# Performance work log

Measured on AMD Instinct MI355X. Metric: run time of the kernel, lower is better.

Reference implementation:

```python
import jax, jax.numpy as jnp
import numpy as np

GROUPS = 32
EPS = 1e-5


def group_norm(x, gamma, beta):
    B, C, D, H, W = x.shape
    xr = x.reshape(B, GROUPS, C // GROUPS, D, H, W)
    mean = xr.mean(axis=(2, 3, 4, 5), keepdims=True)
    var = xr.var(axis=(2, 3, 4, 5), keepdims=True)
    xn = (xr - mean) * jax.lax.rsqrt(var + EPS)
    xn = xn.reshape(B, C, D, H, W)
    return xn * gamma[None, :, None, None, None] + beta[None, :, None, None, None]


def conv1x1(h, w, b):
    # 1x1x1 Conv3d == channel matmul. w: [O, C], b: [O]
    return jnp.einsum('oc,bcdhw->bodhw', w, h) + b[None, :, None, None, None]


def setup_inputs() -> dict:
    key = jax.random.key(0)
    ks = jax.random.split(key, 10)
    B, C, D, H, W = 2, 128, 16, 16, 16
    x = jax.random.normal(ks[0], (B, C, D, H, W), dtype=jnp.float32)
    gn_w = jnp.ones((C,), dtype=jnp.float32)
    gn_b = jnp.zeros((C,), dtype=jnp.float32)
    # xavier_uniform for [C, C, 1, 1, 1] conv: fan_in = fan_out = C
    lim = float(np.sqrt(6.0 / (C + C)))
    wq = jax.random.uniform(ks[1], (C, C), jnp.float32, -lim, lim)
    wk = jax.random.uniform(ks[2], (C, C), jnp.float32, -lim, lim)
    wv = jax.random.uniform(ks[3], (C, C), jnp.float32, -lim, lim)
    wp = jax.random.uniform(ks[4], (C, C), jnp.float32, -lim, lim) * 1e-05
    bq = jnp.zeros((C,), jnp.float32)
    bk = jnp.zeros((C,), jnp.float32)
    bv = jnp.zeros((C,), jnp.float32)
    bp = jnp.zeros((C,), jnp.float32)
    return {"x": x, "gn_w": gn_w, "gn_b": gn_b, "wq": wq, "bq": bq,
            "wk": wk, "bk": bk, "wv": wv, "bv": bv, "wp": wp, "bp": bp}


def reference(x, gn_w, gn_b, wq, bq, wk, bk, wv, bv, wp, bp):
    B, C, D, H, W = x.shape
    N = D * H * W
    h = group_norm(x, gn_w, gn_b)
    q = conv1x1(h, wq, bq)
    k = conv1x1(h, wk, bk)
    v = conv1x1(h, wv, bv)
    q = q.transpose(0, 2, 3, 4, 1).reshape(B, N, C)   # [B, N, C]
    k = k.reshape(B, C, N)                            # [B, C, N]
    v = v.transpose(0, 2, 3, 4, 1).reshape(B, N, C)   # [B, N, C]
    w = jnp.einsum('bnc,bcm->bnm', q, k) * (C ** -0.5)  # [B, N, N]
    w = jax.nn.softmax(w, axis=-1)
    h = jnp.einsum('bnm,bmc->bnc', w, v)              # [B, N, C]
    h = h.reshape(B, D, H, W, C).transpose(0, 4, 1, 2, 3)
    h = conv1x1(h, wp, bp)
    return x + h
```

## Files before the change

### kernel.cpp

```cpp
#include <hip/hip_runtime.h>
#include <math.h>

#define CC 128
#define NN 4096
#define BB 2
#define NGROUPS 32
#define CPG 4
#define GSIZE (CPG*NN)
#define KSPLIT 16

typedef __attribute__((ext_vector_type(8))) __bf16 bf16x8;
typedef __attribute__((ext_vector_type(4))) float floatx4;

__device__ __forceinline__ unsigned short f2bf(float f) {
  union { float f; unsigned u; } v; v.f = f;
  unsigned r = v.u + 0x7fff + ((v.u >> 16) & 1);
  return (unsigned short)(r >> 16);
}
__device__ __forceinline__ float bf2f(unsigned short u) {
  return __uint_as_float(((unsigned)u) << 16);
}


__device__ __forceinline__ void stage_tile(const unsigned short* __restrict__ gtile,
                                           unsigned short* ltile, int w, int lane) {
  #pragma unroll
  for (int j = 0; j < 4; j++) {
    int off = (w*4 + j) * 512;
    __builtin_amdgcn_global_load_lds(
        (const __attribute__((address_space(1))) unsigned int*)(gtile + off + lane*8),
        (__attribute__((address_space(3))) unsigned int*)(ltile + off),
        16, 0, 0);
  }
}

__global__ void gn_stats_kernel(const float* __restrict__ x, float2* __restrict__ stats,
                                const float* __restrict__ wq, const float* __restrict__ wk,
                                const float* __restrict__ wv, const float* __restrict__ wp,
                                unsigned short* __restrict__ wqb, unsigned short* __restrict__ wkb,
                                unsigned short* __restrict__ wvb, unsigned short* __restrict__ wpb) {
  int t = threadIdx.x;
  if (blockIdx.x < 256) {
    int bid = blockIdx.x;
    const float4* base = (const float4*)(x + (size_t)bid * 4096);
    float4 v = base[t];
    float s  = v.x + v.y + v.z + v.w;
    float ss = v.x*v.x + v.y*v.y + v.z*v.z + v.w*v.w;
    #pragma unroll
    for (int off = 1; off < 64; off <<= 1) {
      s  += __shfl_xor(s, off);
      ss += __shfl_xor(ss, off);
    }
    __shared__ float sred[4], ssred[4];
    if ((t & 63) == 0) { sred[t >> 6] = s; ssred[t >> 6] = ss; }
    __syncthreads();
    if (t == 0)
      stats[bid] = make_float2(sred[0]+sred[1]+sred[2]+sred[3],
                               ssred[0]+ssred[1]+ssred[2]+ssred[3]);
  } else {
    const float sc = 0.08838834764831845f;
    int i = (blockIdx.x - 256) * 256 + t;
    int id = i >> 12, local = i & 4095;
    const float* src = id==0 ? wq : id==1 ? wk : id==2 ? wv : wp;
    unsigned short* dst = id==0 ? wqb : id==1 ? wkb : id==2 ? wvb : wpb;
    float s = (id == 0) ? sc : 1.0f;
    float4 v = ((const float4*)src)[local];
    unsigned p0 = (unsigned)f2bf(v.x*s) | ((unsigned)f2bf(v.y*s) << 16);
    unsigned p1 = (unsigned)f2bf(v.z*s) | ((unsigned)f2bf(v.w*s) << 16);
    ((uint2*)dst)[local] = make_uint2(p0, p1);
  }
}

__global__ __launch_bounds__(256, 2) void qkv_kernel(
    const float* __restrict__ x, const float2* __restrict__ stats,
    const float* __restrict__ gamma, const float* __restrict__ beta,
    const unsigned short* __restrict__ wqb, const unsigned short* __restrict__ wkb,
    const unsigned short* __restrict__ wvb,
    const float* __restrict__ bq, const float* __restrict__ bk, const float* __restrict__ bv,
    unsigned short* __restrict__ q, unsigned short* __restrict__ k, unsigned short* __restrict__ v) {
  int b = blockIdx.y, n0 = blockIdx.x * 16;
  __shared__ unsigned short hs[16][130];
  __shared__ unsigned short vs[16][136];
  __shared__ float gm[NGROUPS], gr[NGROUPS], aa[CC], ab[CC];
  int t = threadIdx.x;
  if (t < NGROUPS) {
    float su = 0.f, ssq = 0.f;
    #pragma unroll
    for (int j = 0; j < 4; j++) {
      float2 p = stats[(b*NGROUPS + t)*4 + j];
      su += p.x; ssq += p.y;
    }
    float mean = su * (1.0f/GSIZE);
    float var  = ssq * (1.0f/GSIZE) - mean*mean;
    gm[t] = mean;
    gr[t] = rsqrtf(var + 1e-5f);
  }
  __syncthreads();
  if (t < CC) {
    int g = t >> 2;
    float a = gr[g] * gamma[t];
    aa[t] = a;
    ab[t] = beta[t] - gm[g] * a;
  }
  __syncthreads();
  #pragma unroll
  for (int j = 0; j < 2; j++) {
    int idx = j*256 + t;
    int c = idx >> 2, n4 = idx & 3;
    float4 xv = *(const float4*)(x + ((size_t)b*CC + c)*NN + n0 + n4*4);
    float a = aa[c], bc = ab[c];
    hs[n4*4+0][c] = f2bf(a*xv.x + bc);
    hs[n4*4+1][c] = f2bf(a*xv.y + bc);
    hs[n4*4+2][c] = f2bf(a*xv.z + bc);
    hs[n4*4+3][c] = f2bf(a*xv.w + bc);
  }
  __syncthreads();
  int w = t >> 6, lane = t & 63, quad = lane >> 4, c = lane & 15;
  int o0 = w * 32;
  bf16x8 af[4];
  #pragma unroll
  for (int ks = 0; ks < 4; ks++)
    af[ks] = *(const bf16x8*)&hs[c][ks*32 + quad*8];
  floatx4 aq[2], ak[2], av[2];
  #pragma unroll
  for (int ct = 0; ct < 2; ct++) {
    aq[ct] = (floatx4){0.f,0.f,0.f,0.f};
    ak[ct] = (floatx4){0.f,0.f,0.f,0.f};
    av[ct] = (floatx4){0.f,0.f,0.f,0.f};
  }
  #pragma unroll
  for (int ks = 0; ks < 4; ks++) {
    #pragma unroll
    for (int ct = 0; ct < 2; ct++) {
      size_t woff = (size_t)(o0 + ct*16 + c)*CC + ks*32 + quad*8;
      bf16x8 bq8 = *(const bf16x8*)(wqb + woff);
      bf16x8 bk8 = *(const bf16x8*)(wkb + woff);
      bf16x8 bv8 = *(const bf16x8*)(wvb + woff);
      aq[ct] = __builtin_amdgcn_mfma_f32_16x16x32_bf16(af[ks], bq8, aq[ct], 0, 0, 0);
      ak[ct] = __builtin_amdgcn_mfma_f32_16x16x32_bf16(af[ks], bk8, ak[ct], 0, 0, 0);
      av[ct] = __builtin_amdgcn_mfma_f32_16x16x32_bf16(af[ks], bv8, av[ct], 0, 0, 0);
    }
  }
  {
    const float sc = 0.08838834764831845f;
    size_t base = (size_t)b*NN*CC + (size_t)blockIdx.x*2048 + w*512;
    #pragma unroll
    for (int ct = 0; ct < 2; ct++) {
      float bqi = bq[o0 + ct*16 + c] * sc;
      float bki = bk[o0 + ct*16 + c];
      #pragma unroll
      for (int r = 0; r < 4; r++) {
        int idx = (quad*4 + r)*32 + ct*16 + c;
        q[base + idx] = f2bf(aq[ct][r] + bqi);
        k[base + idx] = f2bf(ak[ct][r] + bki);
      }
    }
  }
  #pragma unroll
  for (int ct = 0; ct < 2; ct++) {
    float bvi = bv[o0 + ct*16 + c];
    #pragma unroll
    for (int r = 0; r < 4; r++)
      vs[quad*4 + r][o0 + ct*16 + c] = f2bf(av[ct][r] + bvi);
  }
  __syncthreads();
  {
    int ch = t >> 1, part = t & 1;
    int mbase = (n0 & 16) + part*8;
    unsigned pk[4];
    #pragma unroll
    for (int j = 0; j < 4; j++) {
      unsigned lo = vs[part*8 + j*2    ][ch];
      unsigned hi = vs[part*8 + j*2 + 1][ch];
      pk[j] = lo | (hi << 16);
    }
    *(uint4*)(v + (size_t)b*NN*CC + ((size_t)(n0 >> 5))*4096 + (ch >> 4)*512
              + (ch & 15)*32 + mbase) = make_uint4(pk[0], pk[1], pk[2], pk[3]);
  }
}

__global__ __launch_bounds__(256, 2) void attn_kernel(
    const unsigned short* __restrict__ qm,
    const unsigned short* __restrict__ km,
    const unsigned short* __restrict__ vm,
    unsigned short* __restrict__ Opart,
    float* __restrict__ lpart) {
  int b    = blockIdx.z;
  int kh   = blockIdx.y;
  int t    = threadIdx.x;
  int w    = t >> 6, lane = t & 63, quad = lane >> 4, c = lane & 15;

  __shared__ unsigned short Kbuf[8192];
  __shared__ unsigned short Vbuf[8192];
  __shared__ unsigned short Pl[4][32][72];

  int fragoff = c*32 + quad*8;

  bf16x8 qa[2][4];
  const unsigned short* qbase = qm + (size_t)b*NN*CC + ((size_t)(blockIdx.x*8 + w*2))*2048;
  #pragma unroll
  for (int rt = 0; rt < 2; rt++)
    #pragma unroll
    for (int ks = 0; ks < 4; ks++)
      qa[rt][ks] = *(const bf16x8*)(qbase + rt*2048 + ks*512 + fragoff);

  floatx4 O[2][8];
  #pragma unroll
  for (int rt = 0; rt < 2; rt++)
    #pragma unroll
    for (int ct = 0; ct < 8; ct++) O[rt][ct] = (floatx4){0.f,0.f,0.f,0.f};
  float lsum[2][4];
  #pragma unroll
  for (int rt = 0; rt < 2; rt++)
    #pragma unroll
    for (int r = 0; r < 4; r++) lsum[rt][r] = 0.f;

  const unsigned short* kt0 = km + (size_t)b*NN*CC + (size_t)kh*(NN/KSPLIT)*CC;
  const unsigned short* vt0 = vm + (size_t)b*NN*CC + (size_t)kh*(NN/KSPLIT)*CC;

  const int ITERS = NN/KSPLIT/64;

  stage_tile(kt0, Kbuf, w, lane);
  stage_tile(vt0, Vbuf, w, lane);
  __syncthreads();

  for (int it = 0; it < ITERS; it++) {
    floatx4 S[2][4];
    #pragma unroll
    for (int rt = 0; rt < 2; rt++)
      #pragma unroll
      for (int ct = 0; ct < 4; ct++) S[rt][ct] = (floatx4){0.f,0.f,0.f,0.f};
    #pragma unroll
    for (int ks = 0; ks < 4; ks++) {
      #pragma unroll
      for (int ct = 0; ct < 4; ct++) {
        bf16x8 kf = *(const bf16x8*)&Kbuf[ct*2048 + ks*512 + fragoff];
        S[0][ct] = __builtin_amdgcn_mfma_f32_16x16x32_bf16(qa[0][ks], kf, S[0][ct], 0, 0, 0);
        S[1][ct] = __builtin_amdgcn_mfma_f32_16x16x32_bf16(qa[1][ks], kf, S[1][ct], 0, 0, 0);
      }
    }
    #pragma unroll
    for (int rt = 0; rt < 2; rt++) {
      #pragma unroll
      for (int ct = 0; ct < 4; ct++) {
        float e0 = __expf(S[rt][ct][0]);
        float e1 = __expf(S[rt][ct][1]);
        float e2 = __expf(S[rt][ct][2]);
        float e3 = __expf(S[rt][ct][3]);
        lsum[rt][0] += e0; lsum[rt][1] += e1;
        lsum[rt][2] += e2; lsum[rt][3] += e3;
        bool odd = (c & 1);
        float s01 = odd ? e0 : e1;
        float g01 = __shfl_xor(s01, 1);
        unsigned lo0 = __float_as_uint(odd ? g01 : e0);
        unsigned hi0 = __float_as_uint(odd ? e1 : g01);
        unsigned p0 = (hi0 & 0xffff0000u) | (lo0 >> 16);
        float s23 = odd ? e2 : e3;
        float g23 = __shfl_xor(s23, 1);
        unsigned lo1 = __float_as_uint(odd ? g23 : e2);
        unsigned hi1 = __float_as_uint(odd ? e3 : g23);
        unsigned p1 = (hi1 & 0xffff0000u) | (lo1 >> 16);
        int colpair = ct*16 + (c & ~1);
        int rowA = rt*16 + quad*4 + (odd ? 1 : 0);
        int rowB = rt*16 + quad*4 + (odd ? 3 : 2);
        *(unsigned*)&Pl[w][rowA][colpair] = p0;
        *(unsigned*)&Pl[w][rowB][colpair] = p1;
      }
    }
    __syncthreads();
    if (it+1 < ITERS) stage_tile(kt0 + (size_t)(it+1)*8192, Kbuf, w, lane);
    #pragma unroll
    for (int ks2 = 0; ks2 < 2; ks2++) {
      bf16x8 pa0 = *(const bf16x8*)(&Pl[w][c     ][ks2*32 + quad*8]);
      bf16x8 pa1 = *(const bf16x8*)(&Pl[w][16 + c][ks2*32 + quad*8]);
      #pragma unroll
      for (int ct = 0; ct < 8; ct++) {
        bf16x8 vf = *(const bf16x8*)&Vbuf[ks2*4096 + ct*512 + fragoff];
        O[0][ct] = __builtin_amdgcn_mfma_f32_16x16x32_bf16(pa0, vf, O[0][ct], 0, 0, 0);
        O[1][ct] = __builtin_amdgcn_mfma_f32_16x16x32_bf16(pa1, vf, O[1][ct], 0, 0, 0);
      }
    }
    __syncthreads();
    if (it+1 < ITERS) stage_tile(vt0 + (size_t)(it+1)*8192, Vbuf, w, lane);
  }

  size_t nbase = (size_t)(kh*BB + b)*NN + blockIdx.x*128 + w*32;
  #pragma unroll
  for (int rt = 0; rt < 2; rt++)
    #pragma unroll
    for (int r = 0; r < 4; r++) {
      float vsum = lsum[rt][r];
      vsum += __shfl_xor(vsum, 1);
      vsum += __shfl_xor(vsum, 2);
      vsum += __shfl_xor(vsum, 4);
      vsum += __shfl_xor(vsum, 8);
      if (c == 0) lpart[nbase + rt*16 + quad*4 + r] = vsum;
    }
  #pragma unroll
  for (int rt = 0; rt < 2; rt++)
    #pragma unroll
    for (int ct = 0; ct < 8; ct++)
      #pragma unroll
      for (int r = 0; r < 4; r++)
        Opart[(nbase + rt*16 + quad*4 + r)*CC + ct*16 + c] = f2bf(O[rt][ct][r]);
}

__global__ __launch_bounds__(256, 2) void combine_kernel(
    const unsigned short* __restrict__ Opart, const float* __restrict__ lpart,
    const unsigned short* __restrict__ wpb, const float* __restrict__ bp,
    const float* __restrict__ x, float* __restrict__ out) {
  int b = blockIdx.y, n0 = blockIdx.x * 16;
  int t = threadIdx.x;
  __shared__ unsigned short hs[16][130];
  __shared__ float ps[16][132];
  __shared__ float linv[16];
  if (t < 16) {
    float l = 0.f;
    #pragma unroll
    for (int kh = 0; kh < KSPLIT; kh++)
      l += lpart[((size_t)(kh*BB + b))*NN + n0 + t];
    linv[t] = 1.f / l;
  }
  __syncthreads();
  {
    int n = t >> 4, ch0 = (t & 15) * 8;
    float acc[8];
    #pragma unroll
    for (int j = 0; j < 8; j++) acc[j] = 0.f;
    #pragma unroll
    for (int kh = 0; kh < KSPLIT; kh++) {
      uint4 a = *(const uint4*)(Opart + ((size_t)(kh*BB + b)*NN + n0 + n)*CC + ch0);
      unsigned uu[4] = {a.x, a.y, a.z, a.w};
      #pragma unroll
      for (int j = 0; j < 4; j++) {
        acc[j*2    ] += bf2f((unsigned short)(uu[j] & 0xffff));
        acc[j*2 + 1] += bf2f((unsigned short)(uu[j] >> 16));
      }
    }
    float li = linv[n];
    #pragma unroll
    for (int j = 0; j < 8; j++) hs[n][ch0 + j] = f2bf(acc[j] * li);
  }
  __syncthreads();
  int w = t >> 6, lane = t & 63, quad = lane >> 4, c = lane & 15;
  int o0 = w * 32;
  floatx4 acc[2];
  #pragma unroll
  for (int ct = 0; ct < 2; ct++) acc[ct] = (floatx4){0.f,0.f,0.f,0.f};
  #pragma unroll
  for (int ks = 0; ks < 4; ks++) {
    bf16x8 af = *(const bf16x8*)&hs[c][ks*32 + quad*8];
    #pragma unroll
    for (int ct = 0; ct < 2; ct++) {
      bf16x8 bfr = *(const bf16x8*)(wpb + (size_t)(o0 + ct*16 + c)*CC + ks*32 + quad*8);
      acc[ct] = __builtin_amdgcn_mfma_f32_16x16x32_bf16(af, bfr, acc[ct], 0, 0, 0);
    }
  }
  #pragma unroll
  for (int ct = 0; ct < 2; ct++)
    #pragma unroll
    for (int r = 0; r < 4; r++)
      ps[quad*4 + r][o0 + ct*16 + c] = acc[ct][r];
  __syncthreads();
  int o = t >> 1, nh = (t & 1) * 8;
  float bi = bp[o];
  const float* xr = x + ((size_t)b*CC + o)*NN + n0 + nh;
  float* orow = out + ((size_t)b*CC + o)*NN + n0 + nh;
  #pragma unroll
  for (int j4 = 0; j4 < 2; j4++) {
    float4 xv = ((const float4*)xr)[j4];
    float4 ov;
    ov.x = xv.x + ps[nh + j4*4 + 0][o] + bi;
    ov.y = xv.y + ps[nh + j4*4 + 1][o] + bi;
    ov.z = xv.z + ps[nh + j4*4 + 2][o] + bi;
    ov.w = xv.w + ps[nh + j4*4 + 3][o] + bi;
    ((float4*)orow)[j4] = ov;
  }
}

extern "C" void kernel_launch(void* const* d_in, const int* in_sizes, int n_in,
                              void* d_out, int out_size, void* d_ws, size_t ws_size,
                              hipStream_t stream) {
  const float* x    = (const float*)d_in[0];
  const float* gn_w = (const float*)d_in[1];
  const float* gn_b = (const float*)d_in[2];
  const float* wq   = (const float*)d_in[3];
  const float* bq   = (const float*)d_in[4];
  const float* wk   = (const float*)d_in[5];
  const float* bk   = (const float*)d_in[6];
  const float* wv   = (const float*)d_in[7];
  const float* bv   = (const float*)d_in[8];
  const float* wp   = (const float*)d_in[9];
  const float* bp   = (const float*)d_in[10];
  float* out = (float*)d_out;

  char* ws = (char*)d_ws;
  float2*         stats = (float2*)(ws);
  unsigned short* wqb   = (unsigned short*)(ws + 8192);
  unsigned short* wkb   = (unsigned short*)(ws + 8192 + 32768);
  unsigned short* wvb   = (unsigned short*)(ws + 8192 + 65536);
  unsigned short* wpb   = (unsigned short*)(ws + 8192 + 98304);
  unsigned short* qb    = (unsigned short*)(ws + 262144);
  unsigned short* kb    = (unsigned short*)(ws + 262144 + 2097152);
  unsigned short* vb    = (unsigned short*)(ws + 262144 + 2*2097152);
  unsigned short* Opart = (unsigned short*)(ws + 6553600);
  float*          lpart = (float*)(ws + 6553600 + 33554432);

  gn_stats_kernel<<<dim3(320), 256, 0, stream>>>(x, stats, wq, wk, wv, wp,
                                                 wqb, wkb, wvb, wpb);
  qkv_kernel     <<<dim3(NN/16, BB), 256, 0, stream>>>(x, stats, gn_w, gn_b,
                                                       wqb, wkb, wvb, bq, bk, bv,
                                                       qb, kb, vb);
  attn_kernel    <<<dim3(NN/128, KSPLIT, BB), 256, 0, stream>>>(qb, kb, vb, Opart, lpart);
  combine_kernel <<<dim3(NN/16, BB), 256, 0, stream>>>(Opart, lpart, wpb, bp, x, out);
}
```

Baseline: 126.1 us.

## Double-buffer K tiles, halve key split, and pack paired bf16 output stores

Double-buffers the K tile in shared memory so the next K tile is staged at the top of each iteration, overlapping its load with the QK^T and PV work. KSPLIT drops from 16 to 8, so each block walks twice as many key tiles and the partial-output buffer and combine pass shrink by half, at the cost of fewer blocks in the attention grid. The final partial-output write now swaps values between neighbouring lanes and stores two bf16 values per 32-bit write instead of one 16-bit store each. The extra K buffer raises shared-memory use per block, which may affect occupancy at two blocks per CU.

```diff
diff --git a/kernel.cpp b/kernel.cpp
--- a/kernel.cpp
+++ b/kernel.cpp
@@ -7,7 +7,7 @@
 #define NGROUPS 32
 #define CPG 4
 #define GSIZE (CPG*NN)
-#define KSPLIT 16
+#define KSPLIT 8
 
 typedef __attribute__((ext_vector_type(8))) __bf16 bf16x8;
 typedef __attribute__((ext_vector_type(4))) float floatx4;
@@ -190,7 +190,7 @@
   int t    = threadIdx.x;
   int w    = t >> 6, lane = t & 63, quad = lane >> 4, c = lane & 15;
 
-  __shared__ unsigned short Kbuf[8192];
+  __shared__ unsigned short Kbuf[2][8192];
   __shared__ unsigned short Vbuf[8192];
   __shared__ unsigned short Pl[4][32][72];
 
@@ -220,11 +220,13 @@
 
   const int ITERS = NN/KSPLIT/64;
 
-  stage_tile(kt0, Kbuf, w, lane);
+  stage_tile(kt0, Kbuf[0], w, lane);
   stage_tile(vt0, Vbuf, w, lane);
   __syncthreads();
 
   for (int it = 0; it < ITERS; it++) {
+    if (it+1 < ITERS) stage_tile(kt0 + (size_t)(it+1)*8192, Kbuf[(it+1)&1], w, lane);
+    const unsigned short* Kcur = Kbuf[it&1];
     floatx4 S[2][4];
     #pragma unroll
     for (int rt = 0; rt < 2; rt++)
@@ -234,7 +236,7 @@
     for (int ks = 0; ks < 4; ks++) {
       #pragma unroll
       for (int ct = 0; ct < 4; ct++) {
-        bf16x8 kf = *(const bf16x8*)&Kbuf[ct*2048 + ks*512 + fragoff];
+        bf16x8 kf = *(const bf16x8*)&Kcur[ct*2048 + ks*512 + fragoff];
         S[0][ct] = __builtin_amdgcn_mfma_f32_16x16x32_bf16(qa[0][ks], kf, S[0][ct], 0, 0, 0);
         S[1][ct] = __builtin_amdgcn_mfma_f32_16x16x32_bf16(qa[1][ks], kf, S[1][ct], 0, 0, 0);
       }
@@ -268,7 +270,6 @@
       }
     }
     __syncthreads();
-    if (it+1 < ITERS) stage_tile(kt0 + (size_t)(it+1)*8192, Kbuf, w, lane);
     #pragma unroll
     for (int ks2 = 0; ks2 < 2; ks2++) {
       bf16x8 pa0 = *(const bf16x8*)(&Pl[w][c     ][ks2*32 + quad*8]);
@@ -296,13 +297,28 @@
       vsum += __shfl_xor(vsum, 8);
       if (c == 0) lpart[nbase + rt*16 + quad*4 + r] = vsum;
     }
-  #pragma unroll
-  for (int rt = 0; rt < 2; rt++)
-    #pragma unroll
-    for (int ct = 0; ct < 8; ct++)
-      #pragma unroll
-      for (int r = 0; r < 4; r++)
-        Opart[(nbase + rt*16 + quad*4 + r)*CC + ct*16 + c] = f2bf(O[rt][ct][r]);
+  bool odd = (c & 1);
+  int colpair = (c & ~1);
+  #pragma unroll
+  for (int rt = 0; rt < 2; rt++) {
+    #pragma unroll
+    for (int ct = 0; ct < 8; ct++) {
+      unsigned u0 = f2bf(O[rt][ct][0]);
+      unsigned u1 = f2bf(O[rt][ct][1]);
+      unsigned u2 = f2bf(O[rt][ct][2]);
+      unsigned u3 = f2bf(O[rt][ct][3]);
+      unsigned s01 = odd ? u0 : u1;
+      unsigned g01 = __shfl_xor((int)s01, 1);
+      unsigned p0 = odd ? (g01 | (u1 << 16)) : (u0 | (g01 << 16));
+      unsigned s23 = odd ? u2 : u3;
+      unsigned g23 = __shfl_xor((int)s23, 1);
+      unsigned p1 = odd ? (g23 | (u3 << 16)) : (u2 | (g23 << 16));
+      int rowA = rt*16 + quad*4 + (odd ? 1 : 0);
+      int rowB = rt*16 + quad*4 + (odd ? 3 : 2);
+      *(unsigned*)(Opart + (nbase + rowA)*CC + ct*16 + colpair) = p0;
+      *(unsigned*)(Opart + (nbase + rowB)*CC + ct*16 + colpair) = p1;
+    }
+  }
 }
 
 __global__ __launch_bounds__(256, 2) void combine_kernel(
@@ -404,7 +420,7 @@
   unsigned short* kb    = (unsigned short*)(ws + 262144 + 2097152);
   unsigned short* vb    = (unsigned short*)(ws + 262144 + 2*2097152);
   unsigned short* Opart = (unsigned short*)(ws + 6553600);
-  float*          lpart = (float*)(ws + 6553600 + 33554432);
+  float*          lpart = (float*)(ws + 6553600 + 16777216);
 
   gn_stats_kernel<<<dim3(320), 256, 0, stream>>>(x, stats, wq, wk, wv, wp,
                                                  wqb, wkb, wvb, wpb);
```

New measurement: 121.8 us. 3.4% less time.
